# Performance work log

Hardware: AMD Instinct MI355X
Metric: run time of the kernel (lower is better)

The kernel has to match this reference:

```python
import jax, jax.numpy as jnp
import numpy as np

N_NODES = 50000
N_EDGES = 800000
IN_DIM = 128
HID = 128
EMB = 128
HORIZON = 64
ACT = 8
N_AGENTS = 1024


def setup_inputs() -> dict:
    key = jax.random.key(0)
    ks = jax.random.split(key, 16)
    sc = lambda fan_in: 1.0 / np.sqrt(fan_in)

    inp = {
        "node_features": jax.random.normal(ks[0], (N_NODES, IN_DIM), dtype=jnp.float32),
        "edge_index": jax.random.randint(ks[1], (2, N_EDGES), 0, N_NODES, dtype=jnp.int64),
        "agent_idx": jax.random.randint(ks[2], (N_AGENTS,), 0, N_NODES, dtype=jnp.int64),
        # GraphConv1: out = lin_rel(sum_j x_j) + lin_root(x); lin_root has no bias
        "W1_rel": jax.random.uniform(ks[3], (HID, IN_DIM), jnp.float32, -sc(IN_DIM), sc(IN_DIM)),
        "b1_rel": jax.random.uniform(ks[4], (HID,), jnp.float32, -sc(IN_DIM), sc(IN_DIM)),
        "W1_root": jax.random.uniform(ks[5], (HID, IN_DIM), jnp.float32, -sc(IN_DIM), sc(IN_DIM)),
        # GraphConv2
        "W2_rel": jax.random.uniform(ks[6], (EMB, HID), jnp.float32, -sc(HID), sc(HID)),
        "b2_rel": jax.random.uniform(ks[7], (EMB,), jnp.float32, -sc(HID), sc(HID)),
        "W2_root": jax.random.uniform(ks[8], (EMB, HID), jnp.float32, -sc(HID), sc(HID)),
        # Policy MLP: Linear(EMB,HID)-ReLU-Linear(HID,HID)-ReLU-Linear(HID,HORIZON*ACT)
        "Wp1": jax.random.uniform(ks[9], (HID, EMB), jnp.float32, -sc(EMB), sc(EMB)),
        "bp1": jax.random.uniform(ks[10], (HID,), jnp.float32, -sc(EMB), sc(EMB)),
        "Wp2": jax.random.uniform(ks[11], (HID, HID), jnp.float32, -sc(HID), sc(HID)),
        "bp2": jax.random.uniform(ks[12], (HID,), jnp.float32, -sc(HID), sc(HID)),
        "Wp3": jax.random.uniform(ks[13], (HORIZON * ACT, HID), jnp.float32, -sc(HID), sc(HID)),
        "bp3": jax.random.uniform(ks[14], (HORIZON * ACT,), jnp.float32, -sc(HID), sc(HID)),
    }
    return inp


def _graph_conv(x, src, dst, W_rel, b_rel, W_root):
    # aggregate neighbor features (sum over incoming edges), then linear
    aggr = jax.ops.segment_sum(x[src], dst, num_segments=N_NODES)  # [N, d_in]
    return aggr @ W_rel.T + b_rel + x @ W_root.T


def reference(node_features, edge_index, agent_idx,
              W1_rel, b1_rel, W1_root, W2_rel, b2_rel, W2_root,
              Wp1, bp1, Wp2, bp2, Wp3, bp3):
    src, dst = edge_index[0], edge_index[1]
    h = jax.nn.relu(_graph_conv(node_features, src, dst, W1_rel, b1_rel, W1_root))
    z = jax.nn.relu(_graph_conv(h, src, dst, W2_rel, b2_rel, W2_root))
    sel = z[agent_idx]  # [A, EMB]
    m = jax.nn.relu(sel @ Wp1.T + bp1)
    m = jax.nn.relu(m @ Wp2.T + bp2)
    traj = m @ Wp3.T + bp3
    return traj.reshape(-1, HORIZON, ACT)
```

## Files before the change

### kernel.cpp

```cpp
#include <hip/hip_runtime.h>

#define NN 50000
#define NE 800000
#define DIM 128
#define NB 196
#define BCAP 4800
#define K1B 100

typedef __attribute__((ext_vector_type(8))) short bf16x8;
typedef __attribute__((ext_vector_type(8))) unsigned short u16x8;
typedef __attribute__((ext_vector_type(4))) float f32x4;

__device__ __forceinline__ unsigned short f2bf(float f) {
    unsigned int u = __builtin_bit_cast(unsigned int, f);
    u += 0x7fffu + ((u >> 16) & 1u);
    return (unsigned short)(u >> 16);
}
__device__ __forceinline__ float bf2f(unsigned int lo16) {
    return __builtin_bit_cast(float, lo16 << 16);
}

__global__ __launch_bounds__(256)
void cvt_x_kernel(const float* __restrict__ s, unsigned short* __restrict__ d) {
    int base = (blockIdx.x * 256 + threadIdx.x) * 8;
    float4 a = *(const float4*)(s + base);
    float4 b = *(const float4*)(s + base + 4);
    u16x8 r;
    r[0] = f2bf(a.x); r[1] = f2bf(a.y); r[2] = f2bf(a.z); r[3] = f2bf(a.w);
    r[4] = f2bf(b.x); r[5] = f2bf(b.y); r[6] = f2bf(b.z); r[7] = f2bf(b.w);
    *(u16x8*)(d + base) = r;
}

__global__ __launch_bounds__(256)
void cvt_w_kernel(const float* __restrict__ s0, const float* __restrict__ s1,
                  const float* __restrict__ s2, const float* __restrict__ s3,
                  unsigned short* __restrict__ d0, unsigned short* __restrict__ d1,
                  unsigned short* __restrict__ d2, unsigned short* __restrict__ d3,
                  int* __restrict__ bcursor) {
    if (blockIdx.x == 0 && threadIdx.x < NB) bcursor[threadIdx.x] = 0;
    int which = blockIdx.x >> 3;
    const float* s = which == 0 ? s0 : which == 1 ? s1 : which == 2 ? s2 : s3;
    unsigned short* d = which == 0 ? d0 : which == 1 ? d1 : which == 2 ? d2 : d3;
    int base = ((blockIdx.x & 7) * 256 + threadIdx.x) * 8;
    float4 a = *(const float4*)(s + base);
    float4 b = *(const float4*)(s + base + 4);
    u16x8 r;
    r[0] = f2bf(a.x); r[1] = f2bf(a.y); r[2] = f2bf(a.z); r[3] = f2bf(a.w);
    r[4] = f2bf(b.x); r[5] = f2bf(b.y); r[6] = f2bf(b.z); r[7] = f2bf(b.w);
    *(u16x8*)(d + base) = r;
}

__global__ __launch_bounds__(256)
void bucket_kernel(const int* __restrict__ src, const int* __restrict__ dst,
                   int* __restrict__ bcursor, unsigned int* __restrict__ bedge) {
    __shared__ int hist[NB];
    __shared__ int base[NB];
    const int t = threadIdx.x;
    const int e0 = blockIdx.x * (NE / K1B);
    const int e1 = e0 + (NE / K1B);
    for (int i = t; i < NB; i += 256) hist[i] = 0;
    __syncthreads();
    for (int e = e0 + t; e < e1; e += 256)
        atomicAdd(&hist[dst[e] >> 8], 1);
    __syncthreads();
    for (int i = t; i < NB; i += 256) {
        base[i] = atomicAdd(&bcursor[i], hist[i]);
        hist[i] = 0;
    }
    __syncthreads();
    for (int e = e0 + t; e < e1; e += 256) {
        int d = dst[e];
        int b = d >> 8;
        int pos = base[b] + atomicAdd(&hist[b], 1);
        if (pos < BCAP)
            bedge[(size_t)b * BCAP + pos] = ((unsigned int)(d & 255) << 16) | (unsigned int)src[e];
    }
}

__global__ __launch_bounds__(256)
void bucket_csr_kernel(const int* __restrict__ bcursor,
                       const unsigned int* __restrict__ bedge,
                       int* __restrict__ eid, int2* __restrict__ off2) {
    __shared__ int cnt[256], start[256], run[256], s[256];
    const int b = blockIdx.x;
    const int t = threadIdx.x;
    int n = bcursor[b];
    if (n > BCAP) n = BCAP;
    cnt[t] = 0; run[t] = 0;
    __syncthreads();
    const unsigned int* be = bedge + (size_t)b * BCAP;
    for (int i = t; i < n; i += 256)
        atomicAdd(&cnt[be[i] >> 16], 1);
    __syncthreads();
    int v = cnt[t];
    s[t] = v;
#pragma unroll
    for (int d = 1; d < 256; d <<= 1) {
        __syncthreads();
        int tmp = (t >= d) ? s[t - d] : 0;
        __syncthreads();
        s[t] += tmp;
    }
    __syncthreads();
    int ex = s[t] - v;
    start[t] = ex;
    off2[b * 256 + t] = make_int2(b * BCAP + ex, b * BCAP + ex + v);
    __syncthreads();
    for (int i = t; i < n; i += 256) {
        unsigned int w = be[i];
        int node = w >> 16;
        int o = atomicAdd(&run[node], 1);
        eid[(size_t)b * BCAP + start[node] + o] = (int)(w & 0xffffu);
    }
}

__global__ __launch_bounds__(256)
void gather_bf16_kernel(const unsigned short* __restrict__ x,
                        const int2* __restrict__ off2,
                        const int* __restrict__ eid,
                        unsigned short* __restrict__ aggr) {
    const int node = blockIdx.x * 4 + (threadIdx.x >> 6);
    const int lane = threadIdx.x & 63;
    const int2 se = off2[node];
    const int s = se.x;
    const int e = se.y;
    float ax = 0.f, ay = 0.f;
    int i = s;
    for (; i + 4 <= e; i += 4) {
        int n0 = eid[i], n1 = eid[i + 1], n2 = eid[i + 2], n3 = eid[i + 3];
        unsigned int v0 = *(const unsigned int*)(x + (size_t)n0 * DIM + lane * 2);
        unsigned int v1 = *(const unsigned int*)(x + (size_t)n1 * DIM + lane * 2);
        unsigned int v2 = *(const unsigned int*)(x + (size_t)n2 * DIM + lane * 2);
        unsigned int v3 = *(const unsigned int*)(x + (size_t)n3 * DIM + lane * 2);
        ax += (bf2f(v0 & 0xffffu) + bf2f(v1 & 0xffffu))
            + (bf2f(v2 & 0xffffu) + bf2f(v3 & 0xffffu));
        ay += (bf2f(v0 >> 16) + bf2f(v1 >> 16)) + (bf2f(v2 >> 16) + bf2f(v3 >> 16));
    }
    for (; i < e; ++i) {
        int n = eid[i];
        unsigned int v = *(const unsigned int*)(x + (size_t)n * DIM + lane * 2);
        ax += bf2f(v & 0xffffu);
        ay += bf2f(v >> 16);
    }
    unsigned int packed = ((unsigned int)f2bf(ay) << 16) | f2bf(ax);
    *(unsigned int*)(aggr + (size_t)node * DIM + lane * 2) = packed;
}

__global__ __launch_bounds__(256)
void conv_mfma_kernel(const unsigned short* __restrict__ A0,
                      const unsigned short* __restrict__ A1,
                      const unsigned short* __restrict__ W0,
                      const unsigned short* __restrict__ W1,
                      const float* __restrict__ bias,
                      unsigned short* __restrict__ Out) {
    __shared__ __align__(16) unsigned short Wl[16384];
    const int tid = threadIdx.x;
    const int wave = tid >> 6;
    const int lane = tid & 63;
    const int m0 = blockIdx.x * 64 + wave * 16;
    const bool active = m0 < NN;
    const int col = lane & 15;
    const int kgrp = lane >> 4;
    const int swz = (col & 7) << 4;

    f32x4 acc[8];
#pragma unroll
    for (int t = 0; t < 8; ++t) acc[t] = (f32x4){0.f, 0.f, 0.f, 0.f};

    for (int mat = 0; mat < 2; ++mat) {
        const unsigned short* A = mat ? A1 : A0;
        const unsigned short* W = mat ? W1 : W0;
        __syncthreads();
#pragma unroll
        for (int i = 0; i < 8; ++i) {
            int chunk = i * 256 + tid;
            int row = chunk >> 4;
            int b = (chunk * 16) ^ ((row & 7) << 4);
            *(uint4*)((char*)Wl + b) = *(const uint4*)(W + chunk * 8);
        }
        __syncthreads();
        if (active) {
            const int arow = m0 + col;
#pragma unroll
            for (int ks = 0; ks < 4; ++ks) {
                bf16x8 afrag = *(const bf16x8*)(A + (size_t)arow * DIM + ks * 32 + kgrp * 8);
                const int kb = ks * 64 + kgrp * 16;
#pragma unroll
                for (int t = 0; t < 8; ++t) {
                    int n = t * 16 + col;
                    int byteoff = (n * 256 + kb) ^ swz;
                    bf16x8 bfrag = *(const bf16x8*)((const char*)Wl + byteoff);
                    acc[t] = __builtin_amdgcn_mfma_f32_16x16x32_bf16(afrag, bfrag, acc[t], 0, 0, 0);
                }
            }
        }
    }
    if (active) {
        const int rgrp = lane >> 4;
#pragma unroll
        for (int t = 0; t < 8; ++t) {
            int n = t * 16 + col;
            float bv = bias[n];
#pragma unroll
            for (int j = 0; j < 4; ++j) {
                float v = fmaxf(acc[t][j] + bv, 0.f);
                int row = m0 + rgrp * 4 + j;
                Out[(size_t)row * DIM + n] = f2bf(v);
            }
        }
    }
}

__global__ __launch_bounds__(256)
void mlp_kernel(const unsigned short* __restrict__ Z,
                const int* __restrict__ agent_idx,
                const float* __restrict__ Wp1, const float* __restrict__ bp1,
                const float* __restrict__ Wp2, const float* __restrict__ bp2,
                const float* __restrict__ Wp3, const float* __restrict__ bp3,
                float* __restrict__ Out) {
    __shared__ __align__(16) float sel[8][132];
    __shared__ __align__(16) float m1[8][132];
    __shared__ __align__(16) float m2[8][132];
    const int tid = threadIdx.x;
    const int ab = blockIdx.x * 8;

    {
        int al = tid >> 5;
        int c = (tid & 31) * 4;
        int node = agent_idx[ab + al];
        ushort4 v = *(const ushort4*)(Z + (size_t)node * DIM + c);
        sel[al][c + 0] = bf2f(v.x); sel[al][c + 1] = bf2f(v.y);
        sel[al][c + 2] = bf2f(v.z); sel[al][c + 3] = bf2f(v.w);
    }
    __syncthreads();
    {
        int o = tid & 127;
        int g = tid >> 7;
        float acc[4] = {0.f, 0.f, 0.f, 0.f};
        for (int k = 0; k < 128; k += 4) {
            float4 w = *(const float4*)(Wp1 + (size_t)o * 128 + k);
#pragma unroll
            for (int a = 0; a < 4; ++a) {
                int aa = g * 4 + a;
                acc[a] += w.x * sel[aa][k] + w.y * sel[aa][k + 1]
                        + w.z * sel[aa][k + 2] + w.w * sel[aa][k + 3];
            }
        }
        float b = bp1[o];
#pragma unroll
        for (int a = 0; a < 4; ++a) m1[g * 4 + a][o] = fmaxf(acc[a] + b, 0.f);
    }
    __syncthreads();
    {
        int o = tid & 127;
        int g = tid >> 7;
        float acc[4] = {0.f, 0.f, 0.f, 0.f};
        for (int k = 0; k < 128; k += 4) {
            float4 w = *(const float4*)(Wp2 + (size_t)o * 128 + k);
#pragma unroll
            for (int a = 0; a < 4; ++a) {
                int aa = g * 4 + a;
                acc[a] += w.x * m1[aa][k] + w.y * m1[aa][k + 1]
                        + w.z * m1[aa][k + 2] + w.w * m1[aa][k + 3];
            }
        }
        float b = bp2[o];
#pragma unroll
        for (int a = 0; a < 4; ++a) m2[g * 4 + a][o] = fmaxf(acc[a] + b, 0.f);
    }
    __syncthreads();
    {
#pragma unroll
        for (int oo = 0; oo < 2; ++oo) {
            int o = tid + oo * 256;
            float acc[8] = {0.f, 0.f, 0.f, 0.f, 0.f, 0.f, 0.f, 0.f};
            for (int k = 0; k < 128; k += 4) {
                float4 w = *(const float4*)(Wp3 + (size_t)o * 128 + k);
#pragma unroll
                for (int a = 0; a < 8; ++a) {
                    acc[a] += w.x * m2[a][k] + w.y * m2[a][k + 1]
                            + w.z * m2[a][k + 2] + w.w * m2[a][k + 3];
                }
            }
            float b = bp3[o];
#pragma unroll
            for (int a = 0; a < 8; ++a)
                Out[(size_t)(ab + a) * 512 + o] = acc[a] + b;
        }
    }
}

extern "C" void kernel_launch(void* const* d_in, const int* in_sizes, int n_in,
                              void* d_out, int out_size, void* d_ws, size_t ws_size,
                              hipStream_t stream) {
    const float* x       = (const float*)d_in[0];
    const int*   edge    = (const int*)d_in[1];
    const int*   src     = edge;
    const int*   dst     = edge + NE;
    const int*   agent   = (const int*)d_in[2];
    const float* W1_rel  = (const float*)d_in[3];
    const float* b1_rel  = (const float*)d_in[4];
    const float* W1_root = (const float*)d_in[5];
    const float* W2_rel  = (const float*)d_in[6];
    const float* b2_rel  = (const float*)d_in[7];
    const float* W2_root = (const float*)d_in[8];
    const float* Wp1     = (const float*)d_in[9];
    const float* bp1     = (const float*)d_in[10];
    const float* Wp2     = (const float*)d_in[11];
    const float* bp2     = (const float*)d_in[12];
    const float* Wp3     = (const float*)d_in[13];
    const float* bp3     = (const float*)d_in[14];
    float* out = (float*)d_out;

    const size_t NNDIM = (size_t)NN * DIM;
    unsigned short* xb  = (unsigned short*)d_ws;
    unsigned short* ab  = xb + NNDIM;
    unsigned short* hb  = ab + NNDIM;
    unsigned short* zb  = hb + NNDIM;
    unsigned short* w1r = zb + NNDIM;
    unsigned short* w1o = w1r + 16384;
    unsigned short* w2r = w1o + 16384;
    unsigned short* w2o = w2r + 16384;
    int2* off2          = (int2*)(w2o + 16384);
    int* bcursor        = (int*)(off2 + NB * 256);
    unsigned int* bedge = (unsigned int*)(bcursor + 200);
    int* eid            = (int*)(bedge + (size_t)NB * BCAP);

    const int conv_blocks = (NN + 63) / 64;
    const int gather_blocks = NN / 4;

    cvt_x_kernel<<<3125, 256, 0, stream>>>(x, xb);
    cvt_w_kernel<<<32, 256, 0, stream>>>(W1_rel, W1_root, W2_rel, W2_root,
                                         w1r, w1o, w2r, w2o, bcursor);

    bucket_kernel<<<K1B, 256, 0, stream>>>(src, dst, bcursor, bedge);
    bucket_csr_kernel<<<NB, 256, 0, stream>>>(bcursor, bedge, eid, off2);

    gather_bf16_kernel<<<gather_blocks, 256, 0, stream>>>(xb, off2, eid, ab);
    conv_mfma_kernel<<<conv_blocks, 256, 0, stream>>>(ab, xb, w1r, w1o, b1_rel, hb);
    gather_bf16_kernel<<<gather_blocks, 256, 0, stream>>>(hb, off2, eid, ab);
    conv_mfma_kernel<<<conv_blocks, 256, 0, stream>>>(ab, hb, w2r, w2o, b2_rel, zb);
    mlp_kernel<<<1024 / 8, 256, 0, stream>>>(zb, agent, Wp1, bp1, Wp2, bp2, Wp3, bp3, out);
}
```

Baseline: 168.4 us.

## Fuse neighbor gather into MFMA conv kernel and merge conversion kernels

The separate gather kernel is folded into the conv kernel. Each wave sums neighbor features for 16 rows into a swizzled LDS tile, and the MFMA stage reads that tile instead of a global aggregate buffer. This drops the aggregate write and read plus two launches. The x and weight conversion kernels are also merged into one launch. The trade-off is that the gather now runs only 782 blocks with each wave handling 16 rows in sequence, so there is less parallelism and latency hiding than in the old 12500-block gather.

After: 294.4 us. +74.8%, slower.

```diff
diff --git a/kernel.cpp b/kernel.cpp
--- a/kernel.cpp
+++ b/kernel.cpp
@@ -21,27 +21,27 @@
 }
 
 __global__ __launch_bounds__(256)
-void cvt_x_kernel(const float* __restrict__ s, unsigned short* __restrict__ d) {
-    int base = (blockIdx.x * 256 + threadIdx.x) * 8;
-    float4 a = *(const float4*)(s + base);
-    float4 b = *(const float4*)(s + base + 4);
-    u16x8 r;
-    r[0] = f2bf(a.x); r[1] = f2bf(a.y); r[2] = f2bf(a.z); r[3] = f2bf(a.w);
-    r[4] = f2bf(b.x); r[5] = f2bf(b.y); r[6] = f2bf(b.z); r[7] = f2bf(b.w);
-    *(u16x8*)(d + base) = r;
-}
-
-__global__ __launch_bounds__(256)
-void cvt_w_kernel(const float* __restrict__ s0, const float* __restrict__ s1,
-                  const float* __restrict__ s2, const float* __restrict__ s3,
-                  unsigned short* __restrict__ d0, unsigned short* __restrict__ d1,
-                  unsigned short* __restrict__ d2, unsigned short* __restrict__ d3,
-                  int* __restrict__ bcursor) {
-    if (blockIdx.x == 0 && threadIdx.x < NB) bcursor[threadIdx.x] = 0;
-    int which = blockIdx.x >> 3;
-    const float* s = which == 0 ? s0 : which == 1 ? s1 : which == 2 ? s2 : s3;
-    unsigned short* d = which == 0 ? d0 : which == 1 ? d1 : which == 2 ? d2 : d3;
-    int base = ((blockIdx.x & 7) * 256 + threadIdx.x) * 8;
+void cvt_all_kernel(const float* __restrict__ x, unsigned short* __restrict__ xb,
+                    const float* __restrict__ s0, const float* __restrict__ s1,
+                    const float* __restrict__ s2, const float* __restrict__ s3,
+                    unsigned short* __restrict__ d0, unsigned short* __restrict__ d1,
+                    unsigned short* __restrict__ d2, unsigned short* __restrict__ d3,
+                    int* __restrict__ bcursor) {
+    const int blk = blockIdx.x;
+    const float* s;
+    unsigned short* d;
+    int base;
+    if (blk < 3125) {
+        s = x; d = xb;
+        base = (blk * 256 + threadIdx.x) * 8;
+    } else {
+        int wb = blk - 3125;
+        if (wb == 0 && threadIdx.x < NB) bcursor[threadIdx.x] = 0;
+        int which = wb >> 3;
+        s = which == 0 ? s0 : which == 1 ? s1 : which == 2 ? s2 : s3;
+        d = which == 0 ? d0 : which == 1 ? d1 : which == 2 ? d2 : d3;
+        base = ((wb & 7) * 256 + threadIdx.x) * 8;
+    }
     float4 a = *(const float4*)(s + base);
     float4 b = *(const float4*)(s + base + 4);
     u16x8 r;
@@ -115,60 +115,63 @@
 }
 
 __global__ __launch_bounds__(256)
-void gather_bf16_kernel(const unsigned short* __restrict__ x,
-                        const int2* __restrict__ off2,
-                        const int* __restrict__ eid,
-                        unsigned short* __restrict__ aggr) {
-    const int node = blockIdx.x * 4 + (threadIdx.x >> 6);
-    const int lane = threadIdx.x & 63;
-    const int2 se = off2[node];
-    const int s = se.x;
-    const int e = se.y;
-    float ax = 0.f, ay = 0.f;
-    int i = s;
-    for (; i + 4 <= e; i += 4) {
-        int n0 = eid[i], n1 = eid[i + 1], n2 = eid[i + 2], n3 = eid[i + 3];
-        unsigned int v0 = *(const unsigned int*)(x + (size_t)n0 * DIM + lane * 2);
-        unsigned int v1 = *(const unsigned int*)(x + (size_t)n1 * DIM + lane * 2);
-        unsigned int v2 = *(const unsigned int*)(x + (size_t)n2 * DIM + lane * 2);
-        unsigned int v3 = *(const unsigned int*)(x + (size_t)n3 * DIM + lane * 2);
-        ax += (bf2f(v0 & 0xffffu) + bf2f(v1 & 0xffffu))
-            + (bf2f(v2 & 0xffffu) + bf2f(v3 & 0xffffu));
-        ay += (bf2f(v0 >> 16) + bf2f(v1 >> 16)) + (bf2f(v2 >> 16) + bf2f(v3 >> 16));
-    }
-    for (; i < e; ++i) {
-        int n = eid[i];
-        unsigned int v = *(const unsigned int*)(x + (size_t)n * DIM + lane * 2);
-        ax += bf2f(v & 0xffffu);
-        ay += bf2f(v >> 16);
-    }
-    unsigned int packed = ((unsigned int)f2bf(ay) << 16) | f2bf(ax);
-    *(unsigned int*)(aggr + (size_t)node * DIM + lane * 2) = packed;
-}
-
-__global__ __launch_bounds__(256)
-void conv_mfma_kernel(const unsigned short* __restrict__ A0,
-                      const unsigned short* __restrict__ A1,
-                      const unsigned short* __restrict__ W0,
-                      const unsigned short* __restrict__ W1,
-                      const float* __restrict__ bias,
-                      unsigned short* __restrict__ Out) {
+void conv_fused_kernel(const unsigned short* __restrict__ X,
+                       const int2* __restrict__ off2,
+                       const int* __restrict__ eid,
+                       const unsigned short* __restrict__ W0,
+                       const unsigned short* __restrict__ W1,
+                       const float* __restrict__ bias,
+                       unsigned short* __restrict__ Out) {
     __shared__ __align__(16) unsigned short Wl[16384];
+    __shared__ __align__(16) unsigned short Ag[8192];
     const int tid = threadIdx.x;
     const int wave = tid >> 6;
     const int lane = tid & 63;
-    const int m0 = blockIdx.x * 64 + wave * 16;
-    const bool active = m0 < NN;
+    const int m0 = blockIdx.x * 64;
+    const bool active = (m0 + wave * 16) < NN;
     const int col = lane & 15;
     const int kgrp = lane >> 4;
-    const int swz = (col & 7) << 4;
+    const int swzb = (col & 7) << 4;
+
+    for (int r = 0; r < 16; ++r) {
+        const int row = wave * 16 + r;
+        const int node = m0 + row;
+        float ax = 0.f, ay = 0.f;
+        if (node < NN) {
+            const int2 se = off2[node];
+            int i = se.x;
+            const int e = se.y;
+            for (; i + 4 <= e; i += 4) {
+                int n0 = eid[i], n1 = eid[i + 1], n2 = eid[i + 2], n3 = eid[i + 3];
+                unsigned int v0 = *(const unsigned int*)(X + (size_t)n0 * DIM + lane * 2);
+                unsigned int v1 = *(const unsigned int*)(X + (size_t)n1 * DIM + lane * 2);
+                unsigned int v2 = *(const unsigned int*)(X + (size_t)n2 * DIM + lane * 2);
+                unsigned int v3 = *(const unsigned int*)(X + (size_t)n3 * DIM + lane * 2);
+                ax += (bf2f(v0 & 0xffffu) + bf2f(v1 & 0xffffu))
+                    + (bf2f(v2 & 0xffffu) + bf2f(v3 & 0xffffu));
+                ay += (bf2f(v0 >> 16) + bf2f(v1 >> 16)) + (bf2f(v2 >> 16) + bf2f(v3 >> 16));
+            }
+            for (; i < e; ++i) {
+                int n = eid[i];
+                unsigned int v = *(const unsigned int*)(X + (size_t)n * DIM + lane * 2);
+                ax += bf2f(v & 0xffffu);
+                ay += bf2f(v >> 16);
+            }
+        }
+        unsigned int packed = ((unsigned int)f2bf(ay) << 16) | f2bf(ax);
+        int byteoff = (row * 256 + lane * 4) ^ ((row & 7) << 4);
+        *(unsigned int*)((char*)Ag + byteoff) = packed;
+    }
 
     f32x4 acc[8];
 #pragma unroll
     for (int t = 0; t < 8; ++t) acc[t] = (f32x4){0.f, 0.f, 0.f, 0.f};
 
+    const int arow = wave * 16 + col;
+    int growx = m0 + arow;
+    if (growx >= NN) growx = 0;
+
     for (int mat = 0; mat < 2; ++mat) {
-        const unsigned short* A = mat ? A1 : A0;
         const unsigned short* W = mat ? W1 : W0;
         __syncthreads();
 #pragma unroll
@@ -180,15 +183,20 @@
         }
         __syncthreads();
         if (active) {
-            const int arow = m0 + col;
 #pragma unroll
             for (int ks = 0; ks < 4; ++ks) {
-                bf16x8 afrag = *(const bf16x8*)(A + (size_t)arow * DIM + ks * 32 + kgrp * 8);
+                bf16x8 afrag;
+                if (mat == 0) {
+                    int aoff = (arow * 256 + ks * 64 + kgrp * 16) ^ ((arow & 7) << 4);
+                    afrag = *(const bf16x8*)((const char*)Ag + aoff);
+                } else {
+                    afrag = *(const bf16x8*)(X + (size_t)growx * DIM + ks * 32 + kgrp * 8);
+                }
                 const int kb = ks * 64 + kgrp * 16;
 #pragma unroll
                 for (int t = 0; t < 8; ++t) {
                     int n = t * 16 + col;
-                    int byteoff = (n * 256 + kb) ^ swz;
+                    int byteoff = (n * 256 + kb) ^ swzb;
                     bf16x8 bfrag = *(const bf16x8*)((const char*)Wl + byteoff);
                     acc[t] = __builtin_amdgcn_mfma_f32_16x16x32_bf16(afrag, bfrag, acc[t], 0, 0, 0);
                 }
@@ -204,7 +212,7 @@
 #pragma unroll
             for (int j = 0; j < 4; ++j) {
                 float v = fmaxf(acc[t][j] + bv, 0.f);
-                int row = m0 + rgrp * 4 + j;
+                int row = m0 + wave * 16 + rgrp * 4 + j;
                 Out[(size_t)row * DIM + n] = f2bf(v);
             }
         }
@@ -314,8 +322,7 @@
 
     const size_t NNDIM = (size_t)NN * DIM;
     unsigned short* xb  = (unsigned short*)d_ws;
-    unsigned short* ab  = xb + NNDIM;
-    unsigned short* hb  = ab + NNDIM;
+    unsigned short* hb  = xb + NNDIM;
     unsigned short* zb  = hb + NNDIM;
     unsigned short* w1r = zb + NNDIM;
     unsigned short* w1o = w1r + 16384;
@@ -327,18 +334,14 @@
     int* eid            = (int*)(bedge + (size_t)NB * BCAP);
 
     const int conv_blocks = (NN + 63) / 64;
-    const int gather_blocks = NN / 4;
-
-    cvt_x_kernel<<<3125, 256, 0, stream>>>(x, xb);
-    cvt_w_kernel<<<32, 256, 0, stream>>>(W1_rel, W1_root, W2_rel, W2_root,
-                                         w1r, w1o, w2r, w2o, bcursor);
+
+    cvt_all_kernel<<<3157, 256, 0, stream>>>(x, xb, W1_rel, W1_root, W2_rel, W2_root,
+                                             w1r, w1o, w2r, w2o, bcursor);
 
     bucket_kernel<<<K1B, 256, 0, stream>>>(src, dst, bcursor, bedge);
     bucket_csr_kernel<<<NB, 256, 0, stream>>>(bcursor, bedge, eid, off2);
 
-    gather_bf16_kernel<<<gather_blocks, 256, 0, stream>>>(xb, off2, eid, ab);
-    conv_mfma_kernel<<<conv_blocks, 256, 0, stream>>>(ab, xb, w1r, w1o, b1_rel, hb);
-    gather_bf16_kernel<<<gather_blocks, 256, 0, stream>>>(hb, off2, eid, ab);
-    conv_mfma_kernel<<<conv_blocks, 256, 0, stream>>>(ab, hb, w2r, w2o, b2_rel, zb);
+    conv_fused_kernel<<<conv_blocks, 256, 0, stream>>>(xb, off2, eid, w1r, w1o, b1_rel, hb);
+    conv_fused_kernel<<<conv_blocks, 256, 0, stream>>>(hb, off2, eid, w2r, w2o, b2_rel, zb);
     mlp_kernel<<<1024 / 8, 256, 0, stream>>>(zb, agent, Wp1, bp1, Wp2, bp2, Wp3, bp3, out);
 }
```

## Widen gather to 16-byte row loads with edge-split lane groups; merge convert kernels

Applied to the files above, without the earlier changes.

The neighbor gather now has each wave split into four lane groups. Each group handles every fourth edge and loads 16 bytes (8 bf16) per lane instead of 4 bytes. Partial sums are combined with cross-lane shuffles, and one group writes the result, which cuts the number of load instructions and adds more edges in flight per node. The x and weight bf16 conversion kernels are also merged into one launch to save a kernel launch. In exchange the gather pays extra shuffle reductions, and its load balance changes for nodes with few edges.

Result: faster. 153.4 us (-8.9%).

```diff
diff --git a/kernel.cpp b/kernel.cpp
--- a/kernel.cpp
+++ b/kernel.cpp
@@ -21,27 +21,27 @@
 }
 
 __global__ __launch_bounds__(256)
-void cvt_x_kernel(const float* __restrict__ s, unsigned short* __restrict__ d) {
-    int base = (blockIdx.x * 256 + threadIdx.x) * 8;
-    float4 a = *(const float4*)(s + base);
-    float4 b = *(const float4*)(s + base + 4);
-    u16x8 r;
-    r[0] = f2bf(a.x); r[1] = f2bf(a.y); r[2] = f2bf(a.z); r[3] = f2bf(a.w);
-    r[4] = f2bf(b.x); r[5] = f2bf(b.y); r[6] = f2bf(b.z); r[7] = f2bf(b.w);
-    *(u16x8*)(d + base) = r;
-}
-
-__global__ __launch_bounds__(256)
-void cvt_w_kernel(const float* __restrict__ s0, const float* __restrict__ s1,
-                  const float* __restrict__ s2, const float* __restrict__ s3,
-                  unsigned short* __restrict__ d0, unsigned short* __restrict__ d1,
-                  unsigned short* __restrict__ d2, unsigned short* __restrict__ d3,
-                  int* __restrict__ bcursor) {
-    if (blockIdx.x == 0 && threadIdx.x < NB) bcursor[threadIdx.x] = 0;
-    int which = blockIdx.x >> 3;
-    const float* s = which == 0 ? s0 : which == 1 ? s1 : which == 2 ? s2 : s3;
-    unsigned short* d = which == 0 ? d0 : which == 1 ? d1 : which == 2 ? d2 : d3;
-    int base = ((blockIdx.x & 7) * 256 + threadIdx.x) * 8;
+void cvt_all_kernel(const float* __restrict__ x, unsigned short* __restrict__ xb,
+                    const float* __restrict__ s0, const float* __restrict__ s1,
+                    const float* __restrict__ s2, const float* __restrict__ s3,
+                    unsigned short* __restrict__ d0, unsigned short* __restrict__ d1,
+                    unsigned short* __restrict__ d2, unsigned short* __restrict__ d3,
+                    int* __restrict__ bcursor) {
+    const int blk = blockIdx.x;
+    const float* s;
+    unsigned short* d;
+    int base;
+    if (blk < 3125) {
+        s = x; d = xb;
+        base = (blk * 256 + threadIdx.x) * 8;
+    } else {
+        int wb = blk - 3125;
+        if (wb == 0 && threadIdx.x < NB) bcursor[threadIdx.x] = 0;
+        int which = wb >> 3;
+        s = which == 0 ? s0 : which == 1 ? s1 : which == 2 ? s2 : s3;
+        d = which == 0 ? d0 : which == 1 ? d1 : which == 2 ? d2 : d3;
+        base = ((wb & 7) * 256 + threadIdx.x) * 8;
+    }
     float4 a = *(const float4*)(s + base);
     float4 b = *(const float4*)(s + base + 4);
     u16x8 r;
@@ -121,29 +121,39 @@
                         unsigned short* __restrict__ aggr) {
     const int node = blockIdx.x * 4 + (threadIdx.x >> 6);
     const int lane = threadIdx.x & 63;
+    const int grp  = lane >> 4;
+    const int c16  = lane & 15;
     const int2 se = off2[node];
-    const int s = se.x;
-    const int e = se.y;
-    float ax = 0.f, ay = 0.f;
-    int i = s;
-    for (; i + 4 <= e; i += 4) {
-        int n0 = eid[i], n1 = eid[i + 1], n2 = eid[i + 2], n3 = eid[i + 3];
-        unsigned int v0 = *(const unsigned int*)(x + (size_t)n0 * DIM + lane * 2);
-        unsigned int v1 = *(const unsigned int*)(x + (size_t)n1 * DIM + lane * 2);
-        unsigned int v2 = *(const unsigned int*)(x + (size_t)n2 * DIM + lane * 2);
-        unsigned int v3 = *(const unsigned int*)(x + (size_t)n3 * DIM + lane * 2);
-        ax += (bf2f(v0 & 0xffffu) + bf2f(v1 & 0xffffu))
-            + (bf2f(v2 & 0xffffu) + bf2f(v3 & 0xffffu));
-        ay += (bf2f(v0 >> 16) + bf2f(v1 >> 16)) + (bf2f(v2 >> 16) + bf2f(v3 >> 16));
-    }
-    for (; i < e; ++i) {
+    const int s = se.x, e = se.y;
+    const unsigned short* __restrict__ xc = x + c16 * 8;
+    float acc[8] = {0.f, 0.f, 0.f, 0.f, 0.f, 0.f, 0.f, 0.f};
+    int i = s + grp;
+    for (; i + 4 < e; i += 8) {
+        int n0 = eid[i];
+        int n1 = eid[i + 4];
+        u16x8 v0 = *(const u16x8*)(xc + (size_t)n0 * DIM);
+        u16x8 v1 = *(const u16x8*)(xc + (size_t)n1 * DIM);
+#pragma unroll
+        for (int j = 0; j < 8; ++j)
+            acc[j] += bf2f((unsigned short)v0[j]) + bf2f((unsigned short)v1[j]);
+    }
+    if (i < e) {
         int n = eid[i];
-        unsigned int v = *(const unsigned int*)(x + (size_t)n * DIM + lane * 2);
-        ax += bf2f(v & 0xffffu);
-        ay += bf2f(v >> 16);
-    }
-    unsigned int packed = ((unsigned int)f2bf(ay) << 16) | f2bf(ax);
-    *(unsigned int*)(aggr + (size_t)node * DIM + lane * 2) = packed;
+        u16x8 v = *(const u16x8*)(xc + (size_t)n * DIM);
+#pragma unroll
+        for (int j = 0; j < 8; ++j) acc[j] += bf2f((unsigned short)v[j]);
+    }
+#pragma unroll
+    for (int j = 0; j < 8; ++j) {
+        acc[j] += __shfl_xor(acc[j], 16, 64);
+        acc[j] += __shfl_xor(acc[j], 32, 64);
+    }
+    if (grp == 0) {
+        u16x8 r;
+#pragma unroll
+        for (int j = 0; j < 8; ++j) r[j] = f2bf(acc[j]);
+        *(u16x8*)(aggr + (size_t)node * DIM + c16 * 8) = r;
+    }
 }
 
 __global__ __launch_bounds__(256)
@@ -329,9 +339,8 @@
     const int conv_blocks = (NN + 63) / 64;
     const int gather_blocks = NN / 4;
 
-    cvt_x_kernel<<<3125, 256, 0, stream>>>(x, xb);
-    cvt_w_kernel<<<32, 256, 0, stream>>>(W1_rel, W1_root, W2_rel, W2_root,
-                                         w1r, w1o, w2r, w2o, bcursor);
+    cvt_all_kernel<<<3157, 256, 0, stream>>>(x, xb, W1_rel, W1_root, W2_rel, W2_root,
+                                             w1r, w1o, w2r, w2o, bcursor);
 
     bucket_kernel<<<K1B, 256, 0, stream>>>(src, dst, bcursor, bedge);
     bucket_csr_kernel<<<NB, 256, 0, stream>>>(bcursor, bedge, eid, off2);
```
